# Kernel tuning notes

Measured on AMD Instinct MI355X. Metric: run time of the kernel, lower is better.

The kernel has to match this reference:

```python
import jax, jax.numpy as jnp
import numpy as np

N_NODES = 50000
N_EDGES = 800000
IN_FEATS = 128
OUT_FEATS = 64


def setup_inputs() -> dict:
    key = jax.random.key(0)
    k1, k2, k3, k4, k5, k6 = jax.random.split(key, 6)
    feat = jax.random.normal(k1, (N_NODES, IN_FEATS), dtype=jnp.float32)
    edge_src = jax.random.randint(k2, (N_EDGES,), 0, N_NODES, dtype=jnp.int64)
    edge_dst = jax.random.randint(k3, (N_EDGES,), 0, N_NODES, dtype=jnp.int64)
    eweight = jax.random.uniform(k4, (N_EDGES,), dtype=jnp.float32)
    W = jax.random.normal(k5, (OUT_FEATS, IN_FEATS), dtype=jnp.float32) * (1.0 / np.sqrt(IN_FEATS))
    b = jax.random.normal(k6, (OUT_FEATS,), dtype=jnp.float32) * 0.01
    return {"feat": feat, "edge_src": edge_src, "edge_dst": edge_dst,
            "eweight": eweight, "W": W, "b": b}


def reference(feat, edge_src, edge_dst, eweight, W, b):
    # Linear: [N, in] @ [in, out] + [out]
    h = jnp.einsum('ni,oi->no', feat, W) + b
    # u_mul_e: gather src features, scale by per-edge weight -> [E, out]
    m = h[edge_src] * eweight[:, None]
    # sum reduce over dst -> [N, out]
    out = jax.ops.segment_sum(m, edge_dst, num_segments=N_NODES)
    return out
```

## Files before the change

### kernel.cpp

```cpp
#include <hip/hip_runtime.h>

#define IN_FEATS 128
#define OUT_FEATS 64
#define TM 64
#define ALD 136
#define BW_LOG 6
#define BWIDTH 64
#define MAX_NB 1024
#define SE_PER_BLK 2048
#define CAP 2048

typedef short bf16x8 __attribute__((ext_vector_type(8)));
typedef float f32x4 __attribute__((ext_vector_type(4)));

__device__ inline unsigned short f2bf(float f) {
    unsigned u = __float_as_uint(f);
    u += 0x7FFFu + ((u >> 16) & 1u);
    return (unsigned short)(u >> 16);
}
__device__ inline float bf2f_lo(unsigned v) { return __uint_as_float(v << 16); }
__device__ inline float bf2f_hi(unsigned v) { return __uint_as_float(v & 0xFFFF0000u); }
__device__ inline ushort4 cvt4(float4 t) {
    ushort4 s; s.x = f2bf(t.x); s.y = f2bf(t.y); s.z = f2bf(t.z); s.w = f2bf(t.w);
    return s;
}

__global__ __launch_bounds__(256) void init_cursors(int* __restrict__ gcur, int nb)
{
    for (int i = threadIdx.x; i < nb; i += 256) gcur[i] = i * CAP;
}

__global__ __launch_bounds__(256) void stage_linear(
    const float* __restrict__ feat, const float* __restrict__ W,
    const float* __restrict__ b, unsigned short* __restrict__ h,
    const int* __restrict__ esrc, const int* __restrict__ edst,
    const float* __restrict__ ew, int* __restrict__ gcur,
    int2* __restrict__ gstage, int n_nodes, int n_edges, int nb, int nstage)
{
    __shared__ union {
        struct { unsigned short As[TM * ALD]; unsigned short Ws[OUT_FEATS * ALD]; } lin;
        struct { int cnt[MAX_NB]; int base[MAX_NB]; } st;
    } sm;
    const int tid = threadIdx.x;

    if ((int)blockIdx.x < nstage) {
        int* cnt  = sm.st.cnt;
        int* base = sm.st.base;
        for (int i = tid; i < nb; i += 256) cnt[i] = 0;
        __syncthreads();

        const int e0 = blockIdx.x * SE_PER_BLK + tid * 8;
        int dk[8]; int sk[8]; float wk[8]; int bk[8]; int rk[8];
        if (e0 + 7 < n_edges) {
            *((int4*)&dk[0]) = *((const int4*)&edst[e0]);
            *((int4*)&dk[4]) = *((const int4*)&edst[e0 + 4]);
            *((int4*)&sk[0]) = *((const int4*)&esrc[e0]);
            *((int4*)&sk[4]) = *((const int4*)&esrc[e0 + 4]);
            *((float4*)&wk[0]) = *((const float4*)&ew[e0]);
            *((float4*)&wk[4]) = *((const float4*)&ew[e0 + 4]);
#pragma unroll
            for (int i = 0; i < 8; ++i) {
                bk[i] = dk[i] >> BW_LOG;
                rk[i] = atomicAdd(&cnt[bk[i]], 1);
            }
        } else {
#pragma unroll
            for (int i = 0; i < 8; ++i) {
                int e = e0 + i;
                if (e < n_edges) {
                    dk[i] = edst[e]; sk[i] = esrc[e]; wk[i] = ew[e];
                    bk[i] = dk[i] >> BW_LOG;
                    rk[i] = atomicAdd(&cnt[bk[i]], 1);
                } else bk[i] = -1;
            }
        }
        __syncthreads();
        for (int i = tid; i < nb; i += 256) {
            int c = cnt[i];
            base[i] = c ? atomicAdd(&gcur[i], c) : 0;
        }
        __syncthreads();
#pragma unroll
        for (int i = 0; i < 8; ++i) {
            if (bk[i] >= 0) {
                int pos = base[bk[i]] + rk[i];
                if (pos < (bk[i] + 1) * CAP)
                    gstage[pos] =
                        make_int2(((dk[i] & (BWIDTH - 1)) << 16) | sk[i],
                                  __float_as_int(wk[i]));
            }
        }
    } else {
        unsigned short* As = sm.lin.As;
        unsigned short* Ws = sm.lin.Ws;
        const int row0 = ((int)blockIdx.x - nstage) * TM;

        {
            const int c  = tid & 63;
            const int kb = (tid >> 6) * 32;
            const float4* wrow = (const float4*)(W + (size_t)c * IN_FEATS + kb);
#pragma unroll
            for (int i = 0; i < 8; ++i)
                *((ushort4*)&Ws[c * ALD + kb + i * 4]) = cvt4(wrow[i]);
        }
        {
#pragma unroll
            for (int i = 0; i < 8; ++i) {
                int flat = i * 256 + tid;
                int r  = flat >> 5;
                int kc = flat & 31;
                int gr = row0 + r;
                float4 t = (gr < n_nodes)
                    ? ((const float4*)(feat + (size_t)gr * IN_FEATS))[kc]
                    : make_float4(0.f, 0.f, 0.f, 0.f);
                *((ushort4*)&As[r * ALD + kc * 4]) = cvt4(t);
            }
        }
        __syncthreads();

        const int w    = tid >> 6;
        const int lane = tid & 63;
        const int m    = lane & 15;
        const int quad = lane >> 4;
        const int koff = quad * 8;

        f32x4 acc[4];
#pragma unroll
        for (int t = 0; t < 4; ++t) acc[t] = (f32x4){0.f, 0.f, 0.f, 0.f};

#pragma unroll
        for (int chunk = 0; chunk < 4; ++chunk) {
            const int kc = chunk * 32 + koff;
            bf16x8 a = *((const bf16x8*)&As[(w * 16 + m) * ALD + kc]);
#pragma unroll
            for (int t = 0; t < 4; ++t) {
                bf16x8 bfr = *((const bf16x8*)&Ws[(t * 16 + m) * ALD + kc]);
                acc[t] = __builtin_amdgcn_mfma_f32_16x16x32_bf16(a, bfr, acc[t], 0, 0, 0);
            }
        }

#pragma unroll
        for (int t = 0; t < 4; ++t) {
            const int col = t * 16 + m;
            const float bias = b[col];
#pragma unroll
            for (int i = 0; i < 4; ++i) {
                int r = row0 + w * 16 + quad * 4 + i;
                if (r < n_nodes)
                    h[(size_t)r * OUT_FEATS + col] = f2bf(acc[t][i] + bias);
            }
        }
    }
}

__global__ __launch_bounds__(512) void sort_gather(
    const unsigned short* __restrict__ h, const int* __restrict__ gcur,
    const int2* __restrict__ gstage, float* __restrict__ out, int n_nodes)
{
    __shared__ int2 recs[CAP];
    __shared__ int2 srec[CAP];
    __shared__ int cnt[BWIDTH];
    __shared__ int cur0[BWIDTH];
    __shared__ int cur[BWIDTH];
    const int tid = threadIdx.x;
    const int b   = blockIdx.x;
    const int s0  = b * CAP;
    const int m   = min(gcur[b] - s0, CAP);

    if (tid < BWIDTH) cnt[tid] = 0;
    __syncthreads();

    for (int i = tid; i < m; i += 512) {
        int2 r = gstage[s0 + i];
        recs[i] = r;
        atomicAdd(&cnt[(r.x >> 16) & 63], 1);
    }
    __syncthreads();

    if (tid < 64) {
        int v = cnt[tid];
        int inc = v;
        for (int o = 1; o < 64; o <<= 1) {
            int t = __shfl_up(inc, o, 64);
            if (tid >= o) inc += t;
        }
        int excl = inc - v;
        cur0[tid] = excl;
        cur[tid]  = excl;
    }
    __syncthreads();

    for (int i = tid; i < m; i += 512) {
        int2 r = recs[i];
        int pos = atomicAdd(&cur[(r.x >> 16) & 63], 1);
        srec[pos] = r;
    }
    __syncthreads();

    const int lane = tid & 63;
    const int wv   = tid >> 6;
    const int g    = lane >> 4;
    const int f4   = lane & 15;
    const uint2* h64 = (const uint2*)h;

#pragma unroll
    for (int it = 0; it < 2; ++it) {
        const int nl   = wv * 8 + it * 4 + g;
        const int node = b * BWIDTH + nl;
        const int st   = cur0[nl];
        const int len  = cnt[nl];
        int omax = len;
        omax = max(omax, __shfl_xor(omax, 16, 64));
        omax = max(omax, __shfl_xor(omax, 32, 64));

        float a0 = 0.f, a1 = 0.f, a2 = 0.f, a3 = 0.f;
        for (int u = 0; u < omax; u += 8) {
            int2 r[8]; uint2 hv[8];
#pragma unroll
            for (int k = 0; k < 8; ++k) {
                int uk = u + k;
                r[k] = srec[(uk < len) ? (st + uk) : 0];
            }
#pragma unroll
            for (int k = 0; k < 8; ++k)
                hv[k] = h64[(size_t)(r[k].x & 0xFFFF) * 16 + f4];
#pragma unroll
            for (int k = 0; k < 8; ++k) {
                float w = (u + k < len) ? __int_as_float(r[k].y) : 0.f;
                a0 += w * bf2f_lo(hv[k].x);
                a1 += w * bf2f_hi(hv[k].x);
                a2 += w * bf2f_lo(hv[k].y);
                a3 += w * bf2f_hi(hv[k].y);
            }
        }
        if (node < n_nodes) {
            float4 o; o.x = a0; o.y = a1; o.z = a2; o.w = a3;
            *((float4*)&out[(size_t)node * OUT_FEATS + f4 * 4]) = o;
        }
    }
}

__global__ __launch_bounds__(256) void scatter_kernel(
    const unsigned short* __restrict__ h, const int* __restrict__ esrc,
    const int* __restrict__ edst, const float* __restrict__ ew,
    float* __restrict__ out, int n_edges)
{
    const int lane = threadIdx.x & 63;
    const int wave = threadIdx.x >> 6;
    const int stride = gridDim.x * 4;
    for (int e = blockIdx.x * 4 + wave; e < n_edges; e += stride) {
        const int s = esrc[e];
        const int d = edst[e];
        const float w = ew[e];
        atomicAdd(out + (size_t)d * OUT_FEATS + lane,
                  bf2f_lo((unsigned)h[(size_t)s * OUT_FEATS + lane]) * w);
    }
}

extern "C" void kernel_launch(void* const* d_in, const int* in_sizes, int n_in,
                              void* d_out, int out_size, void* d_ws, size_t ws_size,
                              hipStream_t stream) {
    const float* feat = (const float*)d_in[0];
    const int*   esrc = (const int*)d_in[1];
    const int*   edst = (const int*)d_in[2];
    const float* ew   = (const float*)d_in[3];
    const float* W    = (const float*)d_in[4];
    const float* b    = (const float*)d_in[5];
    float* out = (float*)d_out;

    const int n_nodes = in_sizes[0] / IN_FEATS;
    const int n_edges = in_sizes[1];
    const int nb = (n_nodes + BWIDTH - 1) >> BW_LOG;
    const int nlin = (n_nodes + TM - 1) / TM;
    const int nstage = (n_edges + SE_PER_BLK - 1) / SE_PER_BLK;

    char* wsb = (char*)d_ws;
    unsigned short* h = (unsigned short*)wsb;
    size_t off_gcur  = (((size_t)n_nodes * OUT_FEATS * sizeof(unsigned short)) + 15) & ~(size_t)15;
    size_t sz_gcur   = (((size_t)nb * sizeof(int)) + 15) & ~(size_t)15;
    size_t off_stage = off_gcur + sz_gcur;
    size_t needed    = off_stage + (size_t)nb * CAP * sizeof(int2);

    bool binnable = (nb <= MAX_NB) && (n_nodes < 65536) &&
                    ((size_t)n_edges / (size_t)nb * 3 / 2 + 300 <= CAP);

    if (ws_size >= needed && binnable) {
        int*  gcur   = (int*)(wsb + off_gcur);
        int2* gstage = (int2*)(wsb + off_stage);
        init_cursors<<<1, 256, 0, stream>>>(gcur, nb);
        stage_linear<<<nstage + nlin, 256, 0, stream>>>(
            feat, W, b, h, esrc, edst, ew, gcur, gstage,
            n_nodes, n_edges, nb, nstage);
        sort_gather<<<nb, 512, 0, stream>>>(h, gcur, gstage, out, n_nodes);
    } else {
        stage_linear<<<nlin, 256, 0, stream>>>(
            feat, W, b, h, esrc, edst, ew, nullptr, nullptr,
            n_nodes, n_edges, nb, 0);
        hipMemsetAsync(d_out, 0, (size_t)out_size * sizeof(float), stream);
        scatter_kernel<<<8192, 256, 0, stream>>>(h, esrc, edst, ew, out, n_edges);
    }
}
```

Before: 125.8 us.

## Replace per-bucket LDS sort with shared-memory atomic accumulation in gather

The gather kernel no longer counting-sorts each bucket's edge records by destination. Instead, 16-lane groups stream records straight from global staging, gather the source features and accumulate into a padded transposed LDS tile with float atomics, then write each bucket's 64 rows out. Bucket cursors become zero-based counts set with a memset rather than an init kernel. This removes the sort passes and their barriers, and avoids wave imbalance from uneven per-node degrees, at the cost of many LDS atomics and a nondeterministic summation order.

```diff
diff --git a/kernel.cpp b/kernel.cpp
--- a/kernel.cpp
+++ b/kernel.cpp
@@ -9,6 +9,7 @@
 #define MAX_NB 1024
 #define SE_PER_BLK 2048
 #define CAP 2048
+#define APAD 65
 
 typedef short bf16x8 __attribute__((ext_vector_type(8)));
 typedef float f32x4 __attribute__((ext_vector_type(4)));
@@ -23,11 +24,6 @@
 __device__ inline ushort4 cvt4(float4 t) {
     ushort4 s; s.x = f2bf(t.x); s.y = f2bf(t.y); s.z = f2bf(t.z); s.w = f2bf(t.w);
     return s;
-}
-
-__global__ __launch_bounds__(256) void init_cursors(int* __restrict__ gcur, int nb)
-{
-    for (int i = threadIdx.x; i < nb; i += 256) gcur[i] = i * CAP;
 }
 
 __global__ __launch_bounds__(256) void stage_linear(
@@ -83,9 +79,9 @@
 #pragma unroll
         for (int i = 0; i < 8; ++i) {
             if (bk[i] >= 0) {
-                int pos = base[bk[i]] + rk[i];
-                if (pos < (bk[i] + 1) * CAP)
-                    gstage[pos] =
+                int off = base[bk[i]] + rk[i];
+                if (off < CAP)
+                    gstage[bk[i] * CAP + off] =
                         make_int2(((dk[i] & (BWIDTH - 1)) << 16) | sk[i],
                                   __float_as_int(wk[i]));
             }
@@ -153,90 +149,88 @@
     }
 }
 
-__global__ __launch_bounds__(512) void sort_gather(
-    const unsigned short* __restrict__ h, const int* __restrict__ gcur,
+__global__ __launch_bounds__(512) void acc_gather(
+    const unsigned short* __restrict__ h, const int* __restrict__ gcnt,
     const int2* __restrict__ gstage, float* __restrict__ out, int n_nodes)
 {
-    __shared__ int2 recs[CAP];
-    __shared__ int2 srec[CAP];
-    __shared__ int cnt[BWIDTH];
-    __shared__ int cur0[BWIDTH];
-    __shared__ int cur[BWIDTH];
+    __shared__ float acc[OUT_FEATS * APAD];
     const int tid = threadIdx.x;
     const int b   = blockIdx.x;
     const int s0  = b * CAP;
-    const int m   = min(gcur[b] - s0, CAP);
-
-    if (tid < BWIDTH) cnt[tid] = 0;
+    const int m   = min(gcnt[b], CAP);
+
+    for (int i = tid; i < OUT_FEATS * APAD; i += 512) acc[i] = 0.f;
     __syncthreads();
 
-    for (int i = tid; i < m; i += 512) {
+    const int grp = tid >> 4;
+    const int l4  = tid & 15;
+    const uint2* h64 = (const uint2*)h;
+
+    int i = grp;
+    for (; i + 96 < m; i += 128) {
+        int2 r0 = gstage[s0 + i];
+        int2 r1 = gstage[s0 + i + 32];
+        int2 r2 = gstage[s0 + i + 64];
+        int2 r3 = gstage[s0 + i + 96];
+        uint2 v0 = h64[(size_t)(r0.x & 0xFFFF) * 16 + l4];
+        uint2 v1 = h64[(size_t)(r1.x & 0xFFFF) * 16 + l4];
+        uint2 v2 = h64[(size_t)(r2.x & 0xFFFF) * 16 + l4];
+        uint2 v3 = h64[(size_t)(r3.x & 0xFFFF) * 16 + l4];
+        {
+            float w = __int_as_float(r0.y);
+            float* ap = &acc[(l4 * 4) * APAD + ((r0.x >> 16) & 63)];
+            atomicAdd(ap,            w * bf2f_lo(v0.x));
+            atomicAdd(ap +     APAD, w * bf2f_hi(v0.x));
+            atomicAdd(ap + 2 * APAD, w * bf2f_lo(v0.y));
+            atomicAdd(ap + 3 * APAD, w * bf2f_hi(v0.y));
+        }
+        {
+            float w = __int_as_float(r1.y);
+            float* ap = &acc[(l4 * 4) * APAD + ((r1.x >> 16) & 63)];
+            atomicAdd(ap,            w * bf2f_lo(v1.x));
+            atomicAdd(ap +     APAD, w * bf2f_hi(v1.x));
+            atomicAdd(ap + 2 * APAD, w * bf2f_lo(v1.y));
+            atomicAdd(ap + 3 * APAD, w * bf2f_hi(v1.y));
+        }
+        {
+            float w = __int_as_float(r2.y);
+            float* ap = &acc[(l4 * 4) * APAD + ((r2.x >> 16) & 63)];
+            atomicAdd(ap,            w * bf2f_lo(v2.x));
+            atomicAdd(ap +     APAD, w * bf2f_hi(v2.x));
+            atomicAdd(ap + 2 * APAD, w * bf2f_lo(v2.y));
+            atomicAdd(ap + 3 * APAD, w * bf2f_hi(v2.y));
+        }
+        {
+            float w = __int_as_float(r3.y);
+            float* ap = &acc[(l4 * 4) * APAD + ((r3.x >> 16) & 63)];
+            atomicAdd(ap,            w * bf2f_lo(v3.x));
+            atomicAdd(ap +     APAD, w * bf2f_hi(v3.x));
+            atomicAdd(ap + 2 * APAD, w * bf2f_lo(v3.y));
+            atomicAdd(ap + 3 * APAD, w * bf2f_hi(v3.y));
+        }
+    }
+    for (; i < m; i += 32) {
         int2 r = gstage[s0 + i];
-        recs[i] = r;
-        atomicAdd(&cnt[(r.x >> 16) & 63], 1);
+        uint2 v = h64[(size_t)(r.x & 0xFFFF) * 16 + l4];
+        float w = __int_as_float(r.y);
+        float* ap = &acc[(l4 * 4) * APAD + ((r.x >> 16) & 63)];
+        atomicAdd(ap,            w * bf2f_lo(v.x));
+        atomicAdd(ap +     APAD, w * bf2f_hi(v.x));
+        atomicAdd(ap + 2 * APAD, w * bf2f_lo(v.y));
+        atomicAdd(ap + 3 * APAD, w * bf2f_hi(v.y));
     }
     __syncthreads();
 
-    if (tid < 64) {
-        int v = cnt[tid];
-        int inc = v;
-        for (int o = 1; o < 64; o <<= 1) {
-            int t = __shfl_up(inc, o, 64);
-            if (tid >= o) inc += t;
-        }
-        int excl = inc - v;
-        cur0[tid] = excl;
-        cur[tid]  = excl;
-    }
-    __syncthreads();
-
-    for (int i = tid; i < m; i += 512) {
-        int2 r = recs[i];
-        int pos = atomicAdd(&cur[(r.x >> 16) & 63], 1);
-        srec[pos] = r;
-    }
-    __syncthreads();
-
-    const int lane = tid & 63;
-    const int wv   = tid >> 6;
-    const int g    = lane >> 4;
-    const int f4   = lane & 15;
-    const uint2* h64 = (const uint2*)h;
-
-#pragma unroll
-    for (int it = 0; it < 2; ++it) {
-        const int nl   = wv * 8 + it * 4 + g;
-        const int node = b * BWIDTH + nl;
-        const int st   = cur0[nl];
-        const int len  = cnt[nl];
-        int omax = len;
-        omax = max(omax, __shfl_xor(omax, 16, 64));
-        omax = max(omax, __shfl_xor(omax, 32, 64));
-
-        float a0 = 0.f, a1 = 0.f, a2 = 0.f, a3 = 0.f;
-        for (int u = 0; u < omax; u += 8) {
-            int2 r[8]; uint2 hv[8];
-#pragma unroll
-            for (int k = 0; k < 8; ++k) {
-                int uk = u + k;
-                r[k] = srec[(uk < len) ? (st + uk) : 0];
-            }
-#pragma unroll
-            for (int k = 0; k < 8; ++k)
-                hv[k] = h64[(size_t)(r[k].x & 0xFFFF) * 16 + f4];
-#pragma unroll
-            for (int k = 0; k < 8; ++k) {
-                float w = (u + k < len) ? __int_as_float(r[k].y) : 0.f;
-                a0 += w * bf2f_lo(hv[k].x);
-                a1 += w * bf2f_hi(hv[k].x);
-                a2 += w * bf2f_lo(hv[k].y);
-                a3 += w * bf2f_hi(hv[k].y);
-            }
-        }
-        if (node < n_nodes) {
-            float4 o; o.x = a0; o.y = a1; o.z = a2; o.w = a3;
-            *((float4*)&out[(size_t)node * OUT_FEATS + f4 * 4]) = o;
-        }
+    const int row  = tid >> 3;
+    const int c0   = (tid & 7) * 8;
+    const int node = b * BWIDTH + row;
+    if (node < n_nodes) {
+        float o[8];
+#pragma unroll
+        for (int k = 0; k < 8; ++k) o[k] = acc[(c0 + k) * APAD + row];
+        float* dst = &out[(size_t)node * OUT_FEATS + c0];
+        *((float4*)dst)       = make_float4(o[0], o[1], o[2], o[3]);
+        *((float4*)(dst + 4)) = make_float4(o[4], o[5], o[6], o[7]);
     }
 }
 
@@ -287,11 +281,11 @@
     if (ws_size >= needed && binnable) {
         int*  gcur   = (int*)(wsb + off_gcur);
         int2* gstage = (int2*)(wsb + off_stage);
-        init_cursors<<<1, 256, 0, stream>>>(gcur, nb);
+        hipMemsetAsync(gcur, 0, (size_t)nb * sizeof(int), stream);
         stage_linear<<<nstage + nlin, 256, 0, stream>>>(
             feat, W, b, h, esrc, edst, ew, gcur, gstage,
             n_nodes, n_edges, nb, nstage);
-        sort_gather<<<nb, 512, 0, stream>>>(h, gcur, gstage, out, n_nodes);
+        acc_gather<<<nb, 512, 0, stream>>>(h, gcur, gstage, out, n_nodes);
     } else {
         stage_linear<<<nlin, 256, 0, stream>>>(
             feat, W, b, h, esrc, edst, ew, nullptr, nullptr,
```

New measurement: 448.2 us. 256% more time.
